# Kernel optimization log

Measured on AMD Instinct MI355X. Metric: run time of the kernel, lower is better.

Reference implementation:

```python
import jax, jax.numpy as jnp
import numpy as np

# Santacoder-style MQA transformer, prefill path (equal-length ragged batch)
B, S, D, H, L, FF, V, P = 2, 1024, 2048, 16, 2, 8192, 32000, 8192
HD = D // H               # head_size = 128
EPS = 1e-5
SCALE = HD ** -0.5


def _ln(x, g, b):
    mu = jnp.mean(x, axis=-1, keepdims=True)
    var = jnp.mean(jnp.square(x - mu), axis=-1, keepdims=True)
    return (x - mu) * jax.lax.rsqrt(var + EPS) * g + b


def setup_inputs() -> dict:
    key = jax.random.key(0)
    ks = jax.random.split(key, 8)
    f = lambda k, shape: jax.random.normal(k, shape, dtype=jnp.float32) * 0.02
    return {
        'input_ids': jax.random.randint(ks[0], (B * S,), 0, V),
        'position_ids': jnp.tile(jnp.arange(S), B),
        'wte': f(ks[1], (V, D)),
        'wpe': f(ks[2], (P, D)),
        'c_attn_w': f(ks[3], (L, D, D + 2 * HD)),
        'c_attn_b': jnp.zeros((L, D + 2 * HD), jnp.float32),
        'c_proj_w': f(ks[4], (L, D, D)),
        'c_proj_b': jnp.zeros((L, D), jnp.float32),
        'ln1_w': jnp.ones((L, D), jnp.float32),
        'ln1_b': jnp.zeros((L, D), jnp.float32),
        'ln2_w': jnp.ones((L, D), jnp.float32),
        'ln2_b': jnp.zeros((L, D), jnp.float32),
        'fc_w': f(ks[5], (L, D, FF)),
        'fc_b': jnp.zeros((L, FF), jnp.float32),
        'mp_w': f(ks[6], (L, FF, D)),
        'mp_b': jnp.zeros((L, D), jnp.float32),
        'lnf_w': jnp.ones((D,), jnp.float32),
        'lnf_b': jnp.zeros((D,), jnp.float32),
    }


def _forward(input_ids, position_ids, wte, wpe, c_attn_w, c_attn_b, c_proj_w,
             c_proj_b, ln1_w, ln1_b, ln2_w, ln2_b, fc_w, fc_b, mp_w, mp_b,
             lnf_w, lnf_b):
    T = input_ids.shape[0]                       # total ragged tokens = B*S
    h = wte[input_ids] + wpe[position_ids]       # [T, D]
    causal = jnp.tril(jnp.ones((S, S), dtype=bool))  # per-sequence causal mask
    residual = None
    for l in range(L):
        # FastLayerNorm: fused residual-add + layernorm
        res = h if residual is None else h + residual
        x = _ln(res, ln1_w[l], ln1_b[l])
        # MQA: one query group of H heads, a single shared KV head
        qkv = x @ c_attn_w[l] + c_attn_b[l]       # [T, D + 2*HD]
        q = qkv[:, :D].reshape(B, S, H, HD)
        k = qkv[:, D:D + HD].reshape(B, S, HD)    # single KV head (broadcast over H)
        v = qkv[:, D + HD:].reshape(B, S, HD)
        scores = jnp.einsum('bqhd,bkd->bhqk', q, k) * SCALE
        scores = jnp.where(causal, scores, jnp.finfo(scores.dtype).min)
        probs = jax.nn.softmax(scores, axis=-1)
        ctx = jnp.einsum('bhqk,bkd->bqhd', probs, v).reshape(T, D)
        attn_out = ctx @ c_proj_w[l] + c_proj_b[l]
        res2 = attn_out + res
        x2 = _ln(res2, ln2_w[l], ln2_b[l])
        # gelu_pytorch_tanh -> tanh-approximate gelu
        mlp = jax.nn.gelu(x2 @ fc_w[l] + fc_b[l], approximate=True) @ mp_w[l] + mp_b[l]
        h, residual = mlp, res2
    return _ln(h + residual, lnf_w, lnf_b)        # [T, D]


def reference(input_ids, position_ids, wte, wpe, c_attn_w, c_attn_b, c_proj_w,
              c_proj_b, ln1_w, ln1_b, ln2_w, ln2_b, fc_w, fc_b, mp_w, mp_b,
              lnf_w, lnf_b):
    return _forward(input_ids, position_ids, wte, wpe, c_attn_w, c_attn_b,
                    c_proj_w, c_proj_b, ln1_w, ln1_b, ln2_w, ln2_b, fc_w,
                    fc_b, mp_w, mp_b, lnf_w, lnf_b)
```

## Files before the change

kernel.cpp:

```cpp
#include <hip/hip_runtime.h>
#include <math.h>


typedef __bf16 bf16x8 __attribute__((ext_vector_type(8)));
typedef __bf16 bf16x4v __attribute__((ext_vector_type(4)));
typedef float floatx4 __attribute__((ext_vector_type(4)));

typedef const __attribute__((address_space(1))) void* gas_ptr;
typedef __attribute__((address_space(3))) void* las_ptr;

__device__ __forceinline__ void glds16(const __bf16* g, __bf16* l) {
  __builtin_amdgcn_global_load_lds((gas_ptr)g, (las_ptr)l, 16, 0, 0);
}

__device__ __forceinline__ float gelu_tanh(float x) {
  float u = 0.7978845608028654f * (x + 0.044715f * x * x * x);
  return 0.5f * x * (1.f + tanhf(u));
}

__global__ __launch_bounds__(256)
void embed_kernel(const int* __restrict__ ids, const int* __restrict__ pos,
                  const float* __restrict__ wte, const float* __restrict__ wpe,
                  float* __restrict__ out)
{
  const int t = blockIdx.x;
  const int id = ids[t], pp = pos[t];
  const float4* a = (const float4*)(wte + (size_t)id * 2048);
  const float4* b = (const float4*)(wpe + (size_t)pp * 2048);
  float4* o = (float4*)(out + (size_t)t * 2048);
#pragma unroll
  for (int j = 0; j < 2; j++) {
    int i = threadIdx.x + j * 256;
    float4 x = a[i], y = b[i];
    x.x += y.x; x.y += y.y; x.z += y.z; x.w += y.w;
    o[i] = x;
  }
}

__global__ __launch_bounds__(256)
void wcvt_kernel(const float* __restrict__ in, __bf16* __restrict__ out,
                 const int K, const int N)
{
  __shared__ __bf16 tile[32][36];
  const int n0 = blockIdx.x * 32, k0 = blockIdx.y * 32;
  const int t = threadIdx.x;
  const int r = t >> 3, c = (t & 7) * 4;
  const float4 v = *(const float4*)&in[(size_t)(k0 + r) * N + n0 + c];
  tile[r][c + 0] = (__bf16)v.x;
  tile[r][c + 1] = (__bf16)v.y;
  tile[r][c + 2] = (__bf16)v.z;
  tile[r][c + 3] = (__bf16)v.w;
  __syncthreads();
  bf16x4v w;
  w.x = tile[c + 0][r]; w.y = tile[c + 1][r];
  w.z = tile[c + 2][r]; w.w = tile[c + 3][r];
  *(bf16x4v*)&out[(size_t)(n0 + r) * K + k0 + c] = w;
}

__global__ __launch_bounds__(256)
void vtr_kernel(const __bf16* __restrict__ qkvb, __bf16* __restrict__ vT)
{
  __shared__ __bf16 tile[32][36];
  const int d0 = blockIdx.x * 32, s0 = blockIdx.y * 32, b = blockIdx.z;
  const int t = threadIdx.x;
  const int r = t >> 3, c = (t & 7) * 4;
  bf16x4v v = *(const bf16x4v*)&qkvb[(size_t)(b * 1024 + s0 + r) * 2304 + 2176 + d0 + c];
  tile[r][c + 0] = v.x; tile[r][c + 1] = v.y;
  tile[r][c + 2] = v.z; tile[r][c + 3] = v.w;
  __syncthreads();
  bf16x4v w;
  w.x = tile[c + 0][r]; w.y = tile[c + 1][r];
  w.z = tile[c + 2][r]; w.w = tile[c + 3][r];
  *(bf16x4v*)&vT[(size_t)b * 131072 + (size_t)(d0 + r) * 1024 + s0 + c] = w;
}

__global__ __launch_bounds__(256)
void ln_red_kernel(const float* __restrict__ p0, const float* __restrict__ p1,
                   const float* __restrict__ p2, const float* __restrict__ p3,
                   const float* __restrict__ cbias, const float* __restrict__ resid,
                   float* __restrict__ res_out, __bf16* __restrict__ out_b,
                   float* __restrict__ out_f,
                   const float* __restrict__ gw, const float* __restrict__ gb)
{
  const int row = blockIdx.x;
  const int tid = threadIdx.x;
  const size_t base = (size_t)row * 2048;
  float4 v[2];
  float s = 0.f, sq = 0.f;
#pragma unroll
  for (int j = 0; j < 2; j++) {
    const int idx = tid + j * 256;
    float4 a = ((const float4*)(p0 + base))[idx];
    if (p1) { float4 t = ((const float4*)(p1 + base))[idx];
      a.x += t.x; a.y += t.y; a.z += t.z; a.w += t.w; }
    if (p2) { float4 t = ((const float4*)(p2 + base))[idx];
      a.x += t.x; a.y += t.y; a.z += t.z; a.w += t.w; }
    if (p3) { float4 t = ((const float4*)(p3 + base))[idx];
      a.x += t.x; a.y += t.y; a.z += t.z; a.w += t.w; }
    if (cbias) { float4 t = ((const float4*)cbias)[idx];
      a.x += t.x; a.y += t.y; a.z += t.z; a.w += t.w; }
    if (resid) { float4 t = ((const float4*)(resid + base))[idx];
      a.x += t.x; a.y += t.y; a.z += t.z; a.w += t.w; }
    if (res_out) ((float4*)(res_out + base))[idx] = a;
    v[j] = a;
    s  += a.x + a.y + a.z + a.w;
    sq += a.x * a.x + a.y * a.y + a.z * a.z + a.w * a.w;
  }
  __shared__ float rs[4], rq[4];
  __shared__ float sh_stats[2];
#pragma unroll
  for (int off = 32; off > 0; off >>= 1) {
    s  += __shfl_down(s, off);
    sq += __shfl_down(sq, off);
  }
  const int lane = tid & 63, wave = tid >> 6;
  if (lane == 0) { rs[wave] = s; rq[wave] = sq; }
  __syncthreads();
  if (tid == 0) {
    float S = rs[0] + rs[1] + rs[2] + rs[3];
    float Q = rq[0] + rq[1] + rq[2] + rq[3];
    float mean = S * (1.f / 2048.f);
    float var  = Q * (1.f / 2048.f) - mean * mean;
    sh_stats[0] = mean;
    sh_stats[1] = rsqrtf(var + 1e-5f);
  }
  __syncthreads();
  const float mean = sh_stats[0], rstd = sh_stats[1];
#pragma unroll
  for (int j = 0; j < 2; j++) {
    const int idx = tid + j * 256;
    float4 a = v[j];
    float4 g4 = ((const float4*)gw)[idx];
    float4 b4 = ((const float4*)gb)[idx];
    float y0 = (a.x - mean) * rstd * g4.x + b4.x;
    float y1 = (a.y - mean) * rstd * g4.y + b4.y;
    float y2 = (a.z - mean) * rstd * g4.z + b4.z;
    float y3 = (a.w - mean) * rstd * g4.w + b4.w;
    if (out_b) {
      bf16x4v w;
      w.x = (__bf16)y0; w.y = (__bf16)y1; w.z = (__bf16)y2; w.w = (__bf16)y3;
      *(bf16x4v*)&out_b[base + (size_t)idx * 4] = w;
    }
    if (out_f) {
      float4 w; w.x = y0; w.y = y1; w.z = y2; w.w = y3;
      ((float4*)(out_f + base))[idx] = w;
    }
  }
}

__global__ __launch_bounds__(256)
void bias_red_bf16_kernel(const float* __restrict__ p0, const float* __restrict__ p1,
                          const float* __restrict__ bias, __bf16* __restrict__ out)
{
  const size_t i = ((size_t)blockIdx.x * 256 + threadIdx.x) * 4;
  const int col = (int)(i % 2304);
  float4 a = *(const float4*)(p0 + i);
  const float4 b = *(const float4*)(p1 + i);
  const float4 c = *(const float4*)(bias + col);
  bf16x4v w;
  w.x = (__bf16)(a.x + b.x + c.x);
  w.y = (__bf16)(a.y + b.y + c.y);
  w.z = (__bf16)(a.z + b.z + c.z);
  w.w = (__bf16)(a.w + b.w + c.w);
  *(bf16x4v*)(out + i) = w;
}

template<int MODE>
__global__ __launch_bounds__(256)
void gemm_bt_kernel(const __bf16* __restrict__ A, const __bf16* __restrict__ Bt,
                    const float* __restrict__ bias, void* __restrict__ Cout,
                    const int M, const int N, const int K, const int Kper)
{
  __shared__ __bf16 As[128 * 32];
  __shared__ __bf16 Bs[128 * 32];
  const int tid  = threadIdx.x;
  const int lane = tid & 63;
  const int wave = tid >> 6;
  const int col  = lane & 15;
  const int quad = lane >> 4;
  const int m0 = blockIdx.y * 128;
  const int n0 = blockIdx.x * 128;
  const int wm = (wave & 1) * 64;
  const int wn = (wave >> 1) * 64;
  const int s  = blockIdx.z;
  floatx4 acc[4][4] = {};

  const int srow = tid >> 2;
  const int scol = (tid & 3) * 8;
  const __bf16* Ag = A  + (size_t)s * Kper + (size_t)(m0 + srow) * K + scol;
  const __bf16* Bg = Bt + (size_t)s * Kper + (size_t)(n0 + srow) * K + scol;
  const size_t rowskip = (size_t)64 * K;

  for (int k0 = 0; k0 < Kper; k0 += 32) {
    glds16(Ag + k0,           As + tid * 8);
    glds16(Ag + k0 + rowskip, As + 2048 + tid * 8);
    glds16(Bg + k0,           Bs + tid * 8);
    glds16(Bg + k0 + rowskip, Bs + 2048 + tid * 8);
    __syncthreads();
    bf16x8 af[4], bf[4];
#pragma unroll
    for (int mi = 0; mi < 4; mi++)
      af[mi] = *(const bf16x8*)&As[(wm + mi * 16 + col) * 32 + quad * 8];
#pragma unroll
    for (int ni = 0; ni < 4; ni++)
      bf[ni] = *(const bf16x8*)&Bs[(wn + ni * 16 + col) * 32 + quad * 8];
#pragma unroll
    for (int mi = 0; mi < 4; mi++)
#pragma unroll
      for (int ni = 0; ni < 4; ni++)
        acc[mi][ni] = __builtin_amdgcn_mfma_f32_16x16x32_bf16(af[mi], bf[ni], acc[mi][ni], 0, 0, 0);
    __syncthreads();
  }

  float* Cp = (MODE == 3) ? ((float*)Cout + (size_t)s * M * N) : (float*)Cout;
#pragma unroll
  for (int ni = 0; ni < 4; ni++) {
    const int cc = n0 + wn + ni * 16 + col;
    const float bv = (MODE == 3) ? 0.f : bias[cc];
#pragma unroll
    for (int mi = 0; mi < 4; mi++) {
#pragma unroll
      for (int r = 0; r < 4; r++) {
        const int rr = m0 + wm + mi * 16 + quad * 4 + r;
        float v = acc[mi][ni][r] + bv;
        if constexpr (MODE == 2) v = gelu_tanh(v);
        if constexpr (MODE == 0 || MODE == 3)
          Cp[(size_t)rr * N + cc] = v;
        else
          ((__bf16*)Cout)[(size_t)rr * N + cc] = (__bf16)v;
      }
    }
  }
}

template<int MODE>
__global__ __launch_bounds__(512, 2)
void gemm256_kernel(const __bf16* __restrict__ A, const __bf16* __restrict__ Bt,
                    const float* __restrict__ bias, void* __restrict__ Cout,
                    const int M, const int N, const int K, const int Kper)
{
  __shared__ alignas(16) __bf16 sm[65536];
  const int tid  = threadIdx.x;
  const int lane = tid & 63;
  const int wave = tid >> 6;
  const int col  = lane & 15;
  const int quad = lane >> 4;
  const int wm = (wave >> 2) * 128;
  const int wn = (wave & 3) * 64;
  const int m0 = blockIdx.y * 256;
  const int n0 = blockIdx.x * 256;
  const int ksplit = blockIdx.z;

  const __bf16* Ag = A  + (size_t)m0 * K + (size_t)ksplit * Kper;
  const __bf16* Bg = Bt + (size_t)n0 * K + (size_t)ksplit * Kper;

  const int sr = tid >> 3;
  const int sc = (((tid & 7) ^ (sr & 7)) * 8);
  const int ld = tid * 8;

  const int roff0 = (((0 | quad) ^ (col & 7)) * 8);
  const int roff1 = (((4 | quad) ^ (col & 7)) * 8);

  const int NT = Kper / 64;

  auto stage = [&](int t, int slot) {
    __bf16* dA = sm + slot * 32768;
    __bf16* dB = dA + 16384;
    const __bf16* gA = Ag + t * 64;
    const __bf16* gB = Bg + t * 64;
#pragma unroll
    for (int i = 0; i < 4; i++)
      glds16(gA + (size_t)(i * 64 + sr) * K + sc, dA + i * 4096 + ld);
#pragma unroll
    for (int i = 0; i < 4; i++)
      glds16(gB + (size_t)(i * 64 + sr) * K + sc, dB + i * 4096 + ld);
  };

  floatx4 acc[8][4] = {};

  stage(0, 0);
  stage(1, 1);
  asm volatile("s_waitcnt vmcnt(8)" ::: "memory");
  __builtin_amdgcn_s_barrier();
  __builtin_amdgcn_sched_barrier(0);

  for (int t = 0; t < NT; t++) {
    const int slot = t & 1;
    const __bf16* As = sm + slot * 32768;
    const __bf16* Bs = As + 16384;
    bf16x8 af[8][2], bf[4][2];
#pragma unroll
    for (int ni = 0; ni < 4; ni++) {
      bf[ni][0] = *(const bf16x8*)&Bs[(wn + ni * 16 + col) * 64 + roff0];
      bf[ni][1] = *(const bf16x8*)&Bs[(wn + ni * 16 + col) * 64 + roff1];
    }
#pragma unroll
    for (int mi = 0; mi < 4; mi++) {
      af[mi][0] = *(const bf16x8*)&As[(wm + mi * 16 + col) * 64 + roff0];
      af[mi][1] = *(const bf16x8*)&As[(wm + mi * 16 + col) * 64 + roff1];
    }
    __builtin_amdgcn_s_setprio(1);
#pragma unroll
    for (int mi = 0; mi < 4; mi++)
#pragma unroll
      for (int ni = 0; ni < 4; ni++)
#pragma unroll
        for (int ks = 0; ks < 2; ks++)
          acc[mi][ni] = __builtin_amdgcn_mfma_f32_16x16x32_bf16(
              af[mi][ks], bf[ni][ks], acc[mi][ni], 0, 0, 0);
    __builtin_amdgcn_s_setprio(0);
#pragma unroll
    for (int mi = 4; mi < 8; mi++) {
      af[mi][0] = *(const bf16x8*)&As[(wm + mi * 16 + col) * 64 + roff0];
      af[mi][1] = *(const bf16x8*)&As[(wm + mi * 16 + col) * 64 + roff1];
    }
    asm volatile("s_waitcnt lgkmcnt(0)" ::: "memory");
    __builtin_amdgcn_s_barrier();
    __builtin_amdgcn_sched_barrier(0);
    if (t + 2 < NT) stage(t + 2, slot);
    __builtin_amdgcn_sched_barrier(0);
    __builtin_amdgcn_s_setprio(1);
#pragma unroll
    for (int mi = 4; mi < 8; mi++)
#pragma unroll
      for (int ni = 0; ni < 4; ni++)
#pragma unroll
        for (int ks = 0; ks < 2; ks++)
          acc[mi][ni] = __builtin_amdgcn_mfma_f32_16x16x32_bf16(
              af[mi][ks], bf[ni][ks], acc[mi][ni], 0, 0, 0);
    __builtin_amdgcn_s_setprio(0);
    if (t + 1 < NT) {
      if (t + 2 < NT)
        asm volatile("s_waitcnt vmcnt(8)" ::: "memory");
      else
        asm volatile("s_waitcnt vmcnt(0)" ::: "memory");
      __builtin_amdgcn_s_barrier();
      __builtin_amdgcn_sched_barrier(0);
    }
  }

  float* Cpf = (MODE == 3) ? ((float*)Cout + (size_t)ksplit * M * N) : (float*)Cout;
#pragma unroll
  for (int ni = 0; ni < 4; ni++) {
    const int cc = n0 + wn + ni * 16 + col;
    const float bv = (MODE == 3) ? 0.f : bias[cc];
#pragma unroll
    for (int mi = 0; mi < 8; mi++) {
#pragma unroll
      for (int r = 0; r < 4; r++) {
        const int rr = m0 + wm + mi * 16 + quad * 4 + r;
        float v = acc[mi][ni][r] + bv;
        if constexpr (MODE == 2) v = gelu_tanh(v);
        if constexpr (MODE == 3)
          Cpf[(size_t)rr * N + cc] = v;
        else
          ((__bf16*)Cout)[(size_t)rr * N + cc] = (__bf16)v;
      }
    }
  }
}

__global__ __launch_bounds__(256)
void flash_kernel(const __bf16* __restrict__ qkv, const __bf16* __restrict__ vT,
                  __bf16* __restrict__ ctx)
{
  const int qt = blockIdx.x, h = blockIdx.y, b = blockIdx.z;
  const int tid  = threadIdx.x;
  const int lane = tid & 63, wave = tid >> 6;
  const int col  = lane & 15, quad = lane >> 4;
  __shared__ __bf16 Qs[64 * 128];
  __shared__ __bf16 Ks[64 * 128];
  __shared__ __bf16 Vs[128 * 64];
  __shared__ __bf16 Ps[4][16 * 64];

#pragma unroll
  for (int p = 0; p < 4; p++) {
    int c = tid + p * 256;
    glds16(qkv + (size_t)(b * 1024 + qt * 64 + (c >> 4)) * 2304 + h * 128 + (c & 15) * 8,
           Qs + c * 8);
  }

  float m_i[4], l_i[4];
  floatx4 o[8] = {};
#pragma unroll
  for (int r = 0; r < 4; r++) { m_i[r] = -1e30f; l_i[r] = 0.f; }

  for (int kt = 0; kt <= qt; kt++) {
    __syncthreads();
#pragma unroll
    for (int p = 0; p < 4; p++) {
      int c = tid + p * 256;
      glds16(qkv + (size_t)(b * 1024 + kt * 64 + (c >> 4)) * 2304 + 2048 + (c & 15) * 8,
             Ks + c * 8);
    }
#pragma unroll
    for (int p = 0; p < 4; p++) {
      int c = tid + p * 256;
      glds16(vT + (size_t)b * 131072 + (size_t)(c >> 3) * 1024 + kt * 64 + (c & 7) * 8,
             Vs + c * 8);
    }
    __syncthreads();

    floatx4 sc[4] = {};
#pragma unroll
    for (int kk = 0; kk < 4; kk++) {
      bf16x8 qa = *(const bf16x8*)&Qs[(wave * 16 + col) * 128 + kk * 32 + quad * 8];
#pragma unroll
      for (int ni = 0; ni < 4; ni++) {
        bf16x8 kb = *(const bf16x8*)&Ks[(ni * 16 + col) * 128 + kk * 32 + quad * 8];
        sc[ni] = __builtin_amdgcn_mfma_f32_16x16x32_bf16(qa, kb, sc[ni], 0, 0, 0);
      }
    }

    const bool diag = (kt == qt);
#pragma unroll
    for (int r = 0; r < 4; r++) {
      const int rowL = wave * 16 + quad * 4 + r;
      float mx = -1e30f;
#pragma unroll
      for (int ni = 0; ni < 4; ni++) {
        float s = sc[ni][r] * 0.08838834764831845f;
        if (diag && (ni * 16 + col) > rowL) s = -1e30f;
        sc[ni][r] = s;
        mx = fmaxf(mx, s);
      }
#pragma unroll
      for (int off = 1; off < 16; off <<= 1) mx = fmaxf(mx, __shfl_xor(mx, off));
      const float mnew = fmaxf(m_i[r], mx);
      const float alpha = __expf(m_i[r] - mnew);
      l_i[r] *= alpha;
      float rsum = 0.f;
#pragma unroll
      for (int ni = 0; ni < 4; ni++) {
        float p = __expf(sc[ni][r] - mnew);
        sc[ni][r] = p;
        rsum += p;
      }
#pragma unroll
      for (int off = 1; off < 16; off <<= 1) rsum += __shfl_xor(rsum, off);
      l_i[r] += rsum;
      m_i[r] = mnew;
#pragma unroll
      for (int nd = 0; nd < 8; nd++) o[nd][r] *= alpha;
    }

    __bf16* Pw = &Ps[wave][0];
#pragma unroll
    for (int r = 0; r < 4; r++)
#pragma unroll
      for (int ni = 0; ni < 4; ni++)
        Pw[(quad * 4 + r) * 64 + ni * 16 + col] = (__bf16)sc[ni][r];

#pragma unroll
    for (int kk = 0; kk < 2; kk++) {
      bf16x8 pa = *(const bf16x8*)&Pw[col * 64 + kk * 32 + quad * 8];
#pragma unroll
      for (int nd = 0; nd < 8; nd++) {
        bf16x8 vb = *(const bf16x8*)&Vs[(nd * 16 + col) * 64 + kk * 32 + quad * 8];
        o[nd] = __builtin_amdgcn_mfma_f32_16x16x32_bf16(pa, vb, o[nd], 0, 0, 0);
      }
    }
  }

#pragma unroll
  for (int r = 0; r < 4; r++) {
    const float inv = 1.f / l_i[r];
    const int row = qt * 64 + wave * 16 + quad * 4 + r;
    const size_t base = (size_t)(b * 1024 + row) * 2048 + h * 128;
#pragma unroll
    for (int nd = 0; nd < 8; nd++)
      ctx[base + nd * 16 + col] = (__bf16)(o[nd][r] * inv);
  }
}

extern "C" void kernel_launch(void* const* d_in, const int* in_sizes, int n_in,
                              void* d_out, int out_size, void* d_ws, size_t ws_size,
                              hipStream_t stream)
{
  (void)in_sizes; (void)n_in; (void)out_size; (void)ws_size;
  const int*   ids = (const int*)d_in[0];
  const int*   pos = (const int*)d_in[1];
  const float* wte = (const float*)d_in[2];
  const float* wpe = (const float*)d_in[3];
  const float* caw = (const float*)d_in[4];
  const float* cab = (const float*)d_in[5];
  const float* cpw = (const float*)d_in[6];
  const float* cpb = (const float*)d_in[7];
  const float* l1w = (const float*)d_in[8];
  const float* l1b = (const float*)d_in[9];
  const float* l2w = (const float*)d_in[10];
  const float* l2b = (const float*)d_in[11];
  const float* fcw = (const float*)d_in[12];
  const float* fcb = (const float*)d_in[13];
  const float* mpw = (const float*)d_in[14];
  const float* mpb = (const float*)d_in[15];
  const float* lfw = (const float*)d_in[16];
  const float* lfb = (const float*)d_in[17];
  float* out = (float*)d_out;

  char* ws = (char*)d_ws;
  float*  resA  = (float*)(ws + 0);
  float*  resB  = (float*)(ws + 16777216);
  __bf16* xb    = (__bf16*)(ws + 33554432);
  __bf16* qkvb  = (__bf16*)(ws + 41943040);
  __bf16* ctxb  = (__bf16*)(ws + 51380224);
  __bf16* vtb   = (__bf16*)(ws + 59768832);
  __bf16* wqkvT = (__bf16*)(ws + 60293120);
  __bf16* wprjT = (__bf16*)(ws + 69730304);
  __bf16* wfcT  = (__bf16*)(ws + 78118912);
  __bf16* wmpT  = (__bf16*)(ws + 111673344);
  char*   arena = ws + 145227776;
  float*  pq    = (float*)arena;
  __bf16* mlp1b = (__bf16*)arena;
  float*  pm    = (float*)(ws + 182976512);

  const size_t MN  = (size_t)2048 * 2048;
  const size_t MNq = (size_t)2048 * 2304;

  embed_kernel<<<2048, 256, 0, stream>>>(ids, pos, wte, wpe, resA);

  for (int l = 0; l < 2; l++) {
    if (l == 0)
      ln_red_kernel<<<2048, 256, 0, stream>>>(
          resA, nullptr, nullptr, nullptr, nullptr, nullptr,
          nullptr, xb, nullptr, l1w, l1b);
    else
      ln_red_kernel<<<2048, 256, 0, stream>>>(
          pm, pm + MN, pm + 2 * MN, pm + 3 * MN, mpb, resB,
          resA, xb, nullptr, l1w + 2048, l1b + 2048);

    wcvt_kernel<<<dim3(72, 64), 256, 0, stream>>>(caw + (size_t)l * 2048 * 2304,
                                                  wqkvT, 2048, 2304);
    gemm_bt_kernel<3><<<dim3(18, 16, 2), 256, 0, stream>>>(
        xb, wqkvT, nullptr, pq, 2048, 2304, 2048, 1024);
    bias_red_bf16_kernel<<<4608, 256, 0, stream>>>(pq, pq + MNq, cab + l * 2304, qkvb);

    vtr_kernel<<<dim3(4, 32, 2), 256, 0, stream>>>(qkvb, vtb);
    flash_kernel<<<dim3(16, 16, 2), 256, 0, stream>>>(qkvb, vtb, ctxb);

    wcvt_kernel<<<dim3(64, 64), 256, 0, stream>>>(cpw + (size_t)l * 2048 * 2048,
                                                  wprjT, 2048, 2048);
    gemm256_kernel<3><<<dim3(8, 8, 4), 512, 0, stream>>>(
        ctxb, wprjT, nullptr, pm, 2048, 2048, 2048, 512);
    ln_red_kernel<<<2048, 256, 0, stream>>>(
        pm, pm + MN, pm + 2 * MN, pm + 3 * MN, cpb + l * 2048, resA,
        resB, xb, nullptr, l2w + l * 2048, l2b + l * 2048);

    wcvt_kernel<<<dim3(256, 64), 256, 0, stream>>>(fcw + (size_t)l * 2048 * 8192,
                                                   wfcT, 2048, 8192);
    gemm256_kernel<2><<<dim3(32, 8, 1), 512, 0, stream>>>(
        xb, wfcT, fcb + l * 8192, mlp1b, 2048, 8192, 2048, 2048);

    wcvt_kernel<<<dim3(64, 256), 256, 0, stream>>>(mpw + (size_t)l * 8192 * 2048,
                                                   wmpT, 8192, 2048);
    gemm256_kernel<3><<<dim3(8, 8, 4), 512, 0, stream>>>(
        mlp1b, wmpT, nullptr, pm, 2048, 2048, 8192, 2048);
  }

  ln_red_kernel<<<2048, 256, 0, stream>>>(
      pm, pm + MN, pm + 2 * MN, pm + 3 * MN, mpb + 2048, resB,
      nullptr, nullptr, out, lfw, lfb);
}
```

Baseline: 1.249 ms.

## Swizzle flash-attention LDS tiles and run QKV GEMM through 256-tile kernel

Two separate changes. In the flash-attention kernel, the Q, K, V and P shared-memory tiles are stored with an XOR swizzle on 16-byte groups, so the MFMA operand reads stop hitting the same LDS banks. Separately, the QKV projection drops the 128-tile split-K GEMM plus its fp32 partial-sum reduction kernel and instead uses the 256-tile GEMM with a fused bias and bf16 output. That removes the fp32 partial traffic and one launch, but only 72 blocks are launched for the QKV GEMM, which may underfill the GPU.

After: 1.198 ms. -4.0%, faster.

```diff
diff --git a/kernel.cpp b/kernel.cpp
--- a/kernel.cpp
+++ b/kernel.cpp
@@ -148,91 +148,6 @@
   }
 }
 
-__global__ __launch_bounds__(256)
-void bias_red_bf16_kernel(const float* __restrict__ p0, const float* __restrict__ p1,
-                          const float* __restrict__ bias, __bf16* __restrict__ out)
-{
-  const size_t i = ((size_t)blockIdx.x * 256 + threadIdx.x) * 4;
-  const int col = (int)(i % 2304);
-  float4 a = *(const float4*)(p0 + i);
-  const float4 b = *(const float4*)(p1 + i);
-  const float4 c = *(const float4*)(bias + col);
-  bf16x4v w;
-  w.x = (__bf16)(a.x + b.x + c.x);
-  w.y = (__bf16)(a.y + b.y + c.y);
-  w.z = (__bf16)(a.z + b.z + c.z);
-  w.w = (__bf16)(a.w + b.w + c.w);
-  *(bf16x4v*)(out + i) = w;
-}
-
-template<int MODE>
-__global__ __launch_bounds__(256)
-void gemm_bt_kernel(const __bf16* __restrict__ A, const __bf16* __restrict__ Bt,
-                    const float* __restrict__ bias, void* __restrict__ Cout,
-                    const int M, const int N, const int K, const int Kper)
-{
-  __shared__ __bf16 As[128 * 32];
-  __shared__ __bf16 Bs[128 * 32];
-  const int tid  = threadIdx.x;
-  const int lane = tid & 63;
-  const int wave = tid >> 6;
-  const int col  = lane & 15;
-  const int quad = lane >> 4;
-  const int m0 = blockIdx.y * 128;
-  const int n0 = blockIdx.x * 128;
-  const int wm = (wave & 1) * 64;
-  const int wn = (wave >> 1) * 64;
-  const int s  = blockIdx.z;
-  floatx4 acc[4][4] = {};
-
-  const int srow = tid >> 2;
-  const int scol = (tid & 3) * 8;
-  const __bf16* Ag = A  + (size_t)s * Kper + (size_t)(m0 + srow) * K + scol;
-  const __bf16* Bg = Bt + (size_t)s * Kper + (size_t)(n0 + srow) * K + scol;
-  const size_t rowskip = (size_t)64 * K;
-
-  for (int k0 = 0; k0 < Kper; k0 += 32) {
-    glds16(Ag + k0,           As + tid * 8);
-    glds16(Ag + k0 + rowskip, As + 2048 + tid * 8);
-    glds16(Bg + k0,           Bs + tid * 8);
-    glds16(Bg + k0 + rowskip, Bs + 2048 + tid * 8);
-    __syncthreads();
-    bf16x8 af[4], bf[4];
-#pragma unroll
-    for (int mi = 0; mi < 4; mi++)
-      af[mi] = *(const bf16x8*)&As[(wm + mi * 16 + col) * 32 + quad * 8];
-#pragma unroll
-    for (int ni = 0; ni < 4; ni++)
-      bf[ni] = *(const bf16x8*)&Bs[(wn + ni * 16 + col) * 32 + quad * 8];
-#pragma unroll
-    for (int mi = 0; mi < 4; mi++)
-#pragma unroll
-      for (int ni = 0; ni < 4; ni++)
-        acc[mi][ni] = __builtin_amdgcn_mfma_f32_16x16x32_bf16(af[mi], bf[ni], acc[mi][ni], 0, 0, 0);
-    __syncthreads();
-  }
-
-  float* Cp = (MODE == 3) ? ((float*)Cout + (size_t)s * M * N) : (float*)Cout;
-#pragma unroll
-  for (int ni = 0; ni < 4; ni++) {
-    const int cc = n0 + wn + ni * 16 + col;
-    const float bv = (MODE == 3) ? 0.f : bias[cc];
-#pragma unroll
-    for (int mi = 0; mi < 4; mi++) {
-#pragma unroll
-      for (int r = 0; r < 4; r++) {
-        const int rr = m0 + wm + mi * 16 + quad * 4 + r;
-        float v = acc[mi][ni][r] + bv;
-        if constexpr (MODE == 2) v = gelu_tanh(v);
-        if constexpr (MODE == 0 || MODE == 3)
-          Cp[(size_t)rr * N + cc] = v;
-        else
-          ((__bf16*)Cout)[(size_t)rr * N + cc] = (__bf16)v;
-      }
-    }
-  }
-}
-
 template<int MODE>
 __global__ __launch_bounds__(512, 2)
 void gemm256_kernel(const __bf16* __restrict__ A, const __bf16* __restrict__ Bt,
@@ -376,7 +291,9 @@
 #pragma unroll
   for (int p = 0; p < 4; p++) {
     int c = tid + p * 256;
-    glds16(qkv + (size_t)(b * 1024 + qt * 64 + (c >> 4)) * 2304 + h * 128 + (c & 15) * 8,
+    int row = c >> 4, s = c & 15;
+    int g = (s & 8) | ((s ^ row) & 7);
+    glds16(qkv + (size_t)(b * 1024 + qt * 64 + row) * 2304 + h * 128 + g * 8,
            Qs + c * 8);
   }
 
@@ -390,13 +307,17 @@
 #pragma unroll
     for (int p = 0; p < 4; p++) {
       int c = tid + p * 256;
-      glds16(qkv + (size_t)(b * 1024 + kt * 64 + (c >> 4)) * 2304 + 2048 + (c & 15) * 8,
+      int row = c >> 4, s = c & 15;
+      int g = (s & 8) | ((s ^ row) & 7);
+      glds16(qkv + (size_t)(b * 1024 + kt * 64 + row) * 2304 + 2048 + g * 8,
              Ks + c * 8);
     }
 #pragma unroll
     for (int p = 0; p < 4; p++) {
       int c = tid + p * 256;
-      glds16(vT + (size_t)b * 131072 + (size_t)(c >> 3) * 1024 + kt * 64 + (c & 7) * 8,
+      int row = c >> 3, s = c & 7;
+      int g = (s ^ row) & 7;
+      glds16(vT + (size_t)b * 131072 + (size_t)row * 1024 + kt * 64 + g * 8,
              Vs + c * 8);
     }
     __syncthreads();
@@ -404,10 +325,13 @@
     floatx4 sc[4] = {};
 #pragma unroll
     for (int kk = 0; kk < 4; kk++) {
-      bf16x8 qa = *(const bf16x8*)&Qs[(wave * 16 + col) * 128 + kk * 32 + quad * 8];
+      const int lg = kk * 4 + quad;
+      const int qrow = wave * 16 + col;
+      bf16x8 qa = *(const bf16x8*)&Qs[qrow * 128 + (((lg & 8) | ((lg ^ qrow) & 7)) * 8)];
 #pragma unroll
       for (int ni = 0; ni < 4; ni++) {
-        bf16x8 kb = *(const bf16x8*)&Ks[(ni * 16 + col) * 128 + kk * 32 + quad * 8];
+        const int krow = ni * 16 + col;
+        bf16x8 kb = *(const bf16x8*)&Ks[krow * 128 + (((lg & 8) | ((lg ^ krow) & 7)) * 8)];
         sc[ni] = __builtin_amdgcn_mfma_f32_16x16x32_bf16(qa, kb, sc[ni], 0, 0, 0);
       }
     }
@@ -446,17 +370,24 @@
 
     __bf16* Pw = &Ps[wave][0];
 #pragma unroll
-    for (int r = 0; r < 4; r++)
-#pragma unroll
-      for (int ni = 0; ni < 4; ni++)
-        Pw[(quad * 4 + r) * 64 + ni * 16 + col] = (__bf16)sc[ni][r];
+    for (int r = 0; r < 4; r++) {
+      const int pr = quad * 4 + r;
+#pragma unroll
+      for (int ni = 0; ni < 4; ni++) {
+        const int pc = ni * 16 + col;
+        const int pcs = (pc & 7) | ((((pc >> 3) ^ pr) & 7) << 3);
+        Pw[pr * 64 + pcs] = (__bf16)sc[ni][r];
+      }
+    }
 
 #pragma unroll
     for (int kk = 0; kk < 2; kk++) {
-      bf16x8 pa = *(const bf16x8*)&Pw[col * 64 + kk * 32 + quad * 8];
+      const int lg = kk * 4 + quad;
+      bf16x8 pa = *(const bf16x8*)&Pw[col * 64 + (((lg ^ col) & 7) * 8)];
 #pragma unroll
       for (int nd = 0; nd < 8; nd++) {
-        bf16x8 vb = *(const bf16x8*)&Vs[(nd * 16 + col) * 64 + kk * 32 + quad * 8];
+        const int vr = nd * 16 + col;
+        bf16x8 vb = *(const bf16x8*)&Vs[vr * 64 + (((lg ^ vr) & 7) * 8)];
         o[nd] = __builtin_amdgcn_mfma_f32_16x16x32_bf16(pa, vb, o[nd], 0, 0, 0);
       }
     }
@@ -510,12 +441,10 @@
   __bf16* wfcT  = (__bf16*)(ws + 78118912);
   __bf16* wmpT  = (__bf16*)(ws + 111673344);
   char*   arena = ws + 145227776;
-  float*  pq    = (float*)arena;
   __bf16* mlp1b = (__bf16*)arena;
   float*  pm    = (float*)(ws + 182976512);
 
   const size_t MN  = (size_t)2048 * 2048;
-  const size_t MNq = (size_t)2048 * 2304;
 
   embed_kernel<<<2048, 256, 0, stream>>>(ids, pos, wte, wpe, resA);
 
@@ -531,9 +460,8 @@
 
     wcvt_kernel<<<dim3(72, 64), 256, 0, stream>>>(caw + (size_t)l * 2048 * 2304,
                                                   wqkvT, 2048, 2304);
-    gemm_bt_kernel<3><<<dim3(18, 16, 2), 256, 0, stream>>>(
-        xb, wqkvT, nullptr, pq, 2048, 2304, 2048, 1024);
-    bias_red_bf16_kernel<<<4608, 256, 0, stream>>>(pq, pq + MNq, cab + l * 2304, qkvb);
+    gemm256_kernel<1><<<dim3(9, 8, 1), 512, 0, stream>>>(
+        xb, wqkvT, cab + l * 2304, qkvb, 2048, 2304, 2048, 2048);
 
     vtr_kernel<<<dim3(4, 32, 2), 256, 0, stream>>>(qkvb, vtb);
     flash_kernel<<<dim3(16, 16, 2), 256, 0, stream>>>(qkvb, vtb, ctxb);
```
